# Optimization experiments

Hardware: AMD Instinct MI355X
Metric: run time of the kernel (lower is better)

## Reference

```python
import jax, jax.numpy as jnp
import numpy as np

EPS = 1e-5

def _act_quant(x):
    # per-token int8 absmax quantization (BitNet b1.58)
    scale = 127.0 / jnp.clip(jnp.max(jnp.abs(x), axis=-1, keepdims=True), EPS)
    return jnp.clip(jnp.round(x * scale), -128.0, 127.0) / scale

def _weight_quant(w):
    # per-tensor ternary quantization: round(w/mean|w|) clipped to {-1,0,1}
    scale = 1.0 / jnp.clip(jnp.mean(jnp.abs(w)), EPS)
    return jnp.clip(jnp.round(w * scale), -1.0, 1.0) / scale

def _ste(x, q):
    # straight-through estimator: forward uses q, backward passes through x
    return x + jax.lax.stop_gradient(q - x)

def bitlinear(x, w):
    xq = _ste(x, _act_quant(x))
    wq = _ste(w, _weight_quant(w))
    return jnp.einsum('btd,hd->bth', xq, wq)

def setup_inputs() -> dict:
    key = jax.random.key(0)
    k1, k2, k3 = jax.random.split(key, 3)
    B, T, D, H = 4, 1024, 2048, 8192
    x = jax.random.normal(k1, (B, T, D), dtype=jnp.float32)
    w1 = jax.random.normal(k2, (H, D), dtype=jnp.float32) * 0.02
    w2 = jax.random.normal(k3, (D, H), dtype=jnp.float32) * 0.02
    return {"x": x, "w1": w1, "w2": w2}

def reference(x, w1, w2):
    h = jax.nn.relu(bitlinear(x, w1))   # [B, T, H]
    out = bitlinear(h, w2)              # [B, T, D]
    return out
```

## Files before the change

kernel.cpp:

```cpp
#include <hip/hip_runtime.h>
#include <hip/hip_bf16.h>

#define EPSF 1e-5f

typedef int v4i __attribute__((ext_vector_type(4)));

static constexpr int BB = 4, TT = 1024, DD = 2048, HH = 8192;
static constexpr int MROWS = BB * TT;
static constexpr long long WCOUNT = (long long)DD * HH;


__device__ __forceinline__ void async_copy16(const void* g, void* l) {
  __builtin_amdgcn_global_load_lds(
      (const __attribute__((address_space(1))) unsigned int*)g,
      (__attribute__((address_space(3))) unsigned int*)l,
      16, 0, 0);
}

__device__ __forceinline__ int pack4(float a, float b, float c, float d,
                                     float scale, float lo, float hi) {
  int ia = (int)fminf(fmaxf(rintf(a * scale), lo), hi);
  int ib = (int)fminf(fmaxf(rintf(b * scale), lo), hi);
  int ic = (int)fminf(fmaxf(rintf(c * scale), lo), hi);
  int id = (int)fminf(fmaxf(rintf(d * scale), lo), hi);
  return (ia & 0xff) | ((ib & 0xff) << 8) | ((ic & 0xff) << 16) | ((id & 0xff) << 24);
}

__device__ __forceinline__ float blockMax256(float v) {
  #pragma unroll
  for (int off = 32; off; off >>= 1) v = fmaxf(v, __shfl_down(v, off, 64));
  __shared__ float sm[4];
  int lane = threadIdx.x & 63, wv = threadIdx.x >> 6;
  if (lane == 0) sm[wv] = v;
  __syncthreads();
  return fmaxf(fmaxf(sm[0], sm[1]), fmaxf(sm[2], sm[3]));
}


__global__ __launch_bounds__(256) void abs_sum_kernel(
    const float* __restrict__ w1, const float* __restrict__ w2,
    double* __restrict__ sums) {
  const float* w = blockIdx.y ? w2 : w1;
  const float4* w4 = (const float4*)w;
  long long n4 = WCOUNT / 4;
  float s = 0.f;
  for (long long i = (long long)blockIdx.x * blockDim.x + threadIdx.x; i < n4;
       i += (long long)gridDim.x * blockDim.x) {
    float4 v = w4[i];
    s += fabsf(v.x) + fabsf(v.y) + fabsf(v.z) + fabsf(v.w);
  }
  #pragma unroll
  for (int off = 32; off; off >>= 1) s += __shfl_down(s, off, 64);
  __shared__ float sm[4];
  int lane = threadIdx.x & 63, wv = threadIdx.x >> 6;
  if (lane == 0) sm[wv] = s;
  __syncthreads();
  if (threadIdx.x == 0) {
    float t = sm[0] + sm[1] + sm[2] + sm[3];
    atomicAdd(&sums[blockIdx.y], (double)t);
  }
}


__global__ __launch_bounds__(256) void quant_w_kernel(
    const float* __restrict__ w1, const float* __restrict__ w2,
    const double* __restrict__ sums,
    signed char* __restrict__ q1, signed char* __restrict__ q2) {
  const float* w = blockIdx.y ? w2 : w1;
  signed char* q = blockIdx.y ? q2 : q1;
  float mean = fmaxf((float)(sums[blockIdx.y] * (1.0 / (double)WCOUNT)), EPSF);
  float scale = 1.0f / mean;
  const float4* w4 = (const float4*)w;
  int* q4 = (int*)q;
  long long n4 = WCOUNT / 4;
  for (long long i = (long long)blockIdx.x * blockDim.x + threadIdx.x; i < n4;
       i += (long long)gridDim.x * blockDim.x) {
    float4 v = w4[i];
    q4[i] = pack4(v.x, v.y, v.z, v.w, scale, -1.f, 1.f);
  }
}


__global__ __launch_bounds__(256) void quant_x_kernel(
    const float* __restrict__ x, signed char* __restrict__ xq,
    float* __restrict__ ascale) {
  int row = blockIdx.x;
  const float4* xr = (const float4*)(x + (size_t)row * DD);
  int t = threadIdx.x;
  float4 v0 = xr[2 * t], v1 = xr[2 * t + 1];
  float m = fmaxf(fmaxf(fabsf(v0.x), fabsf(v0.y)), fmaxf(fabsf(v0.z), fabsf(v0.w)));
  m = fmaxf(m, fmaxf(fmaxf(fabsf(v1.x), fabsf(v1.y)), fmaxf(fabsf(v1.z), fabsf(v1.w))));
  float am = fmaxf(blockMax256(m), EPSF);
  float scale = 127.0f / am;
  int* out = (int*)(xq + (size_t)row * DD);
  out[2 * t]     = pack4(v0.x, v0.y, v0.z, v0.w, scale, -128.f, 127.f);
  out[2 * t + 1] = pack4(v1.x, v1.y, v1.z, v1.w, scale, -128.f, 127.f);
  if (t == 0) ascale[row] = am / 127.0f;
}


__global__ __launch_bounds__(256) void quant_h_kernel(
    const float* __restrict__ h, signed char* __restrict__ hq,
    float* __restrict__ ascale) {
  int row = blockIdx.x;
  const float4* hr = (const float4*)(h + (size_t)row * HH);
  int t = threadIdx.x;
  float4 v[8];
  float m = 0.f;
  #pragma unroll
  for (int i = 0; i < 8; i++) {
    v[i] = hr[t + i * 256];
    m = fmaxf(m, fmaxf(fmaxf(fabsf(v[i].x), fabsf(v[i].y)),
                       fmaxf(fabsf(v[i].z), fabsf(v[i].w))));
  }
  float am = fmaxf(blockMax256(m), EPSF);
  float scale = 127.0f / am;
  int* out = (int*)(hq + (size_t)row * HH);
  #pragma unroll
  for (int i = 0; i < 8; i++)
    out[t + i * 256] = pack4(v[i].x, v[i].y, v[i].z, v[i].w, scale, -128.f, 127.f);
  if (t == 0) ascale[row] = am / 127.0f;
}


template <int RELU>
__global__ __launch_bounds__(256) void gemm_i8_kernel(
    const signed char* __restrict__ A, const signed char* __restrict__ B,
    float* __restrict__ C, const float* __restrict__ ascale,
    const double* __restrict__ wsum, int M, int N, int K) {
  __shared__ signed char As[128 * 128];
  __shared__ signed char Bs[128 * 128];

  const int t = threadIdx.x;
  const int lane = t & 63, wv = t >> 6;
  const int wm = wv >> 1, wn = wv & 1;
  const int m0 = blockIdx.y * 128, n0 = blockIdx.x * 128;
  const int q = lane >> 4;

  const int segBase = wv * 4;
  const signed char* aSrc[4];
  const signed char* bSrc[4];
  #pragma unroll
  for (int i = 0; i < 4; i++) {
    int seg = segBase + i;
    int r = seg * 8 + (lane >> 3);
    int c = (lane & 7) ^ (r & 7);
    aSrc[i] = A + (size_t)(m0 + r) * K + c * 16;
    bSrc[i] = B + (size_t)(n0 + r) * K + c * 16;
  }

  v4i acc[4][4];
  #pragma unroll
  for (int i = 0; i < 4; i++)
    #pragma unroll
    for (int j = 0; j < 4; j++) {
      v4i z = {0, 0, 0, 0};
      acc[i][j] = z;
    }

  int rowA[4], rowB[4];
  #pragma unroll
  for (int i = 0; i < 4; i++) {
    rowA[i] = wm * 64 + i * 16 + (lane & 15);
    rowB[i] = wn * 64 + i * 16 + (lane & 15);
  }

  for (int k0 = 0; k0 < K; k0 += 128) {
    #pragma unroll
    for (int i = 0; i < 4; i++) {
      async_copy16(aSrc[i] + k0, &As[(segBase + i) * 1024]);
      async_copy16(bSrc[i] + k0, &Bs[(segBase + i) * 1024]);
    }
    __syncthreads();
    #pragma unroll
    for (int kc = 0; kc < 2; kc++) {
      v4i af[4], bf[4];
      #pragma unroll
      for (int i = 0; i < 4; i++) {
        int ca = (kc * 4 + q) ^ (rowA[i] & 7);
        af[i] = *(const v4i*)(As + rowA[i] * 128 + ca * 16);
        int cb = (kc * 4 + q) ^ (rowB[i] & 7);
        bf[i] = *(const v4i*)(Bs + rowB[i] * 128 + cb * 16);
      }
      #pragma unroll
      for (int i = 0; i < 4; i++)
        #pragma unroll
        for (int j = 0; j < 4; j++)
          acc[i][j] = __builtin_amdgcn_mfma_i32_16x16x64_i8(af[i], bf[j], acc[i][j], 0, 0, 0);
    }
    __syncthreads();
  }

  float wmean = fmaxf((float)(wsum[0] * (1.0 / (double)WCOUNT)), EPSF);
  #pragma unroll
  for (int i = 0; i < 4; i++) {
    int mBase = m0 + wm * 64 + i * 16 + q * 4;
    #pragma unroll
    for (int e = 0; e < 4; e++) {
      float f = ascale[mBase + e] * wmean;
      #pragma unroll
      for (int j = 0; j < 4; j++) {
        int n = n0 + wn * 64 + j * 16 + (lane & 15);
        float v = (float)acc[i][j][e] * f;
        if (RELU) v = fmaxf(v, 0.f);
        C[(size_t)(mBase + e) * N + n] = v;
      }
    }
  }
}


extern "C" void kernel_launch(void* const* d_in, const int* in_sizes, int n_in,
                              void* d_out, int out_size, void* d_ws, size_t ws_size,
                              hipStream_t stream) {
  const float* x  = (const float*)d_in[0];
  const float* w1 = (const float*)d_in[1];
  const float* w2 = (const float*)d_in[2];
  float* out = (float*)d_out;

  char* ws = (char*)d_ws;
  double* sums = (double*)ws;
  float* a1 = (float*)(ws + 256);
  float* a2 = (float*)(ws + 256 + 16384);
  signed char* w1q = (signed char*)(ws + 33024);
  signed char* w2q = w1q + (size_t)WCOUNT;
  signed char* xq  = w2q + (size_t)WCOUNT;
  signed char* hq  = xq + (size_t)MROWS * DD;
  float* h = (float*)(hq + (size_t)MROWS * HH);

  hipMemsetAsync(sums, 0, 16, stream);
  abs_sum_kernel<<<dim3(1024, 2), 256, 0, stream>>>(w1, w2, sums);
  quant_w_kernel<<<dim3(2048, 2), 256, 0, stream>>>(w1, w2, sums, w1q, w2q);
  quant_x_kernel<<<MROWS, 256, 0, stream>>>(x, xq, a1);
  gemm_i8_kernel<1><<<dim3(HH / 128, MROWS / 128), 256, 0, stream>>>(
      xq, w1q, h, a1, &sums[0], MROWS, HH, DD);
  quant_h_kernel<<<MROWS, 256, 0, stream>>>(h, hq, a2);
  gemm_i8_kernel<0><<<dim3(DD / 128, MROWS / 128), 256, 0, stream>>>(
      hq, w2q, out, a2, &sums[1], MROWS, DD, HH);
}
```

Before: 419.1 us.

## Store first GEMM output as int16, add tile swizzle and larger BK

The first GEMM now writes the ReLU'd raw int32 accumulator clamped to int16 rather than scaled float32, which halves the intermediate h write and read traffic. The per-row scale is reapplied inside the h-quantization kernel, which also computes its absmax on integers. It also adds a grouped tile-index swizzle for better L2 reuse and uses a K-tile of 256 for the second GEMM to cut iterations and barriers. Clamping at 32767 can saturate large accumulators and change results, and the larger LDS tile may reduce occupancy.

```diff
diff --git a/kernel.cpp b/kernel.cpp
--- a/kernel.cpp
+++ b/kernel.cpp
@@ -4,6 +4,7 @@
 #define EPSF 1e-5f
 
 typedef int v4i __attribute__((ext_vector_type(4)));
+typedef short v8s __attribute__((ext_vector_type(8)));
 
 static constexpr int BB = 4, TT = 1024, DD = 2048, HH = 8192;
 static constexpr int MROWS = BB * TT;
@@ -26,7 +27,7 @@
   return (ia & 0xff) | ((ib & 0xff) << 8) | ((ic & 0xff) << 16) | ((id & 0xff) << 24);
 }
 
-__device__ __forceinline__ float blockMax256(float v) {
+__device__ __forceinline__ float blockMaxF256(float v) {
   #pragma unroll
   for (int off = 32; off; off >>= 1) v = fmaxf(v, __shfl_down(v, off, 64));
   __shared__ float sm[4];
@@ -34,6 +35,27 @@
   if (lane == 0) sm[wv] = v;
   __syncthreads();
   return fmaxf(fmaxf(sm[0], sm[1]), fmaxf(sm[2], sm[3]));
+}
+
+__device__ __forceinline__ int blockMaxI256(int v) {
+  #pragma unroll
+  for (int off = 32; off; off >>= 1) v = max(v, __shfl_down(v, off, 64));
+  __shared__ int sm[4];
+  int lane = threadIdx.x & 63, wv = threadIdx.x >> 6;
+  if (lane == 0) sm[wv] = v;
+  __syncthreads();
+  return max(max(sm[0], sm[1]), max(sm[2], sm[3]));
+}
+
+__device__ __forceinline__ void swizzle_tiles(int& mt, int& nt) {
+  int Mt = gridDim.y, Nt = gridDim.x;
+  int id = blockIdx.y * Nt + blockIdx.x;
+  int c = id & 7, k = id >> 3;
+  int pm = (Mt >= Nt) ? 4 : 2;
+  int PM = Mt / pm, PN = Nt / (8 / pm);
+  int pr = c % pm, pc = c / pm;
+  mt = pr * PM + (k % PM);
+  nt = pc * PN + (k / PM);
 }
 
 
@@ -90,7 +112,7 @@
   float4 v0 = xr[2 * t], v1 = xr[2 * t + 1];
   float m = fmaxf(fmaxf(fabsf(v0.x), fabsf(v0.y)), fmaxf(fabsf(v0.z), fabsf(v0.w)));
   m = fmaxf(m, fmaxf(fmaxf(fabsf(v1.x), fabsf(v1.y)), fmaxf(fabsf(v1.z), fabsf(v1.w))));
-  float am = fmaxf(blockMax256(m), EPSF);
+  float am = fmaxf(blockMaxF256(m), EPSF);
   float scale = 127.0f / am;
   int* out = (int*)(xq + (size_t)row * DD);
   out[2 * t]     = pack4(v0.x, v0.y, v0.z, v0.w, scale, -128.f, 127.f);
@@ -100,51 +122,66 @@
 
 
 __global__ __launch_bounds__(256) void quant_h_kernel(
-    const float* __restrict__ h, signed char* __restrict__ hq,
-    float* __restrict__ ascale) {
+    const short* __restrict__ h, signed char* __restrict__ hq,
+    float* __restrict__ a2, const float* __restrict__ a1,
+    const double* __restrict__ sums) {
   int row = blockIdx.x;
-  const float4* hr = (const float4*)(h + (size_t)row * HH);
   int t = threadIdx.x;
-  float4 v[8];
-  float m = 0.f;
-  #pragma unroll
-  for (int i = 0; i < 8; i++) {
+  const v8s* hr = (const v8s*)(h + (size_t)row * HH);
+  v8s v[4];
+  int mx = 0;
+  #pragma unroll
+  for (int i = 0; i < 4; i++) {
     v[i] = hr[t + i * 256];
-    m = fmaxf(m, fmaxf(fmaxf(fabsf(v[i].x), fabsf(v[i].y)),
-                       fmaxf(fabsf(v[i].z), fabsf(v[i].w))));
-  }
-  float am = fmaxf(blockMax256(m), EPSF);
+    #pragma unroll
+    for (int j = 0; j < 8; j++) mx = max(mx, (int)v[i][j]);
+  }
+  int bmx = blockMaxI256(mx);
+  float wmean1 = fmaxf((float)(sums[0] * (1.0 / (double)WCOUNT)), EPSF);
+  float f = a1[row] * wmean1;
+  float maxh = (float)bmx * f;
+  float am = fmaxf(maxh, EPSF);
   float scale = 127.0f / am;
   int* out = (int*)(hq + (size_t)row * HH);
   #pragma unroll
-  for (int i = 0; i < 8; i++)
-    out[t + i * 256] = pack4(v[i].x, v[i].y, v[i].z, v[i].w, scale, -128.f, 127.f);
-  if (t == 0) ascale[row] = am / 127.0f;
-}
-
-
-template <int RELU>
+  for (int i = 0; i < 4; i++) {
+    out[(t + i * 256) * 2] =
+        pack4((float)v[i][0] * f, (float)v[i][1] * f, (float)v[i][2] * f,
+              (float)v[i][3] * f, scale, -128.f, 127.f);
+    out[(t + i * 256) * 2 + 1] =
+        pack4((float)v[i][4] * f, (float)v[i][5] * f, (float)v[i][6] * f,
+              (float)v[i][7] * f, scale, -128.f, 127.f);
+  }
+  if (t == 0) a2[row] = am / 127.0f;
+}
+
+
+template <int MODE, int BK>
 __global__ __launch_bounds__(256) void gemm_i8_kernel(
     const signed char* __restrict__ A, const signed char* __restrict__ B,
-    float* __restrict__ C, const float* __restrict__ ascale,
+    void* __restrict__ Cout, const float* __restrict__ ascale,
     const double* __restrict__ wsum, int M, int N, int K) {
-  __shared__ signed char As[128 * 128];
-  __shared__ signed char Bs[128 * 128];
+  constexpr int CH = BK / 16;
+  constexpr int SEGROWS = 1024 / BK;
+  constexpr int SPW = BK / 32;
+  __shared__ signed char As[128 * BK];
+  __shared__ signed char Bs[128 * BK];
 
   const int t = threadIdx.x;
   const int lane = t & 63, wv = t >> 6;
   const int wm = wv >> 1, wn = wv & 1;
-  const int m0 = blockIdx.y * 128, n0 = blockIdx.x * 128;
+  int mt, nt;
+  swizzle_tiles(mt, nt);
+  const int m0 = mt * 128, n0 = nt * 128;
   const int q = lane >> 4;
 
-  const int segBase = wv * 4;
-  const signed char* aSrc[4];
-  const signed char* bSrc[4];
-  #pragma unroll
-  for (int i = 0; i < 4; i++) {
-    int seg = segBase + i;
-    int r = seg * 8 + (lane >> 3);
-    int c = (lane & 7) ^ (r & 7);
+  const signed char* aSrc[SPW];
+  const signed char* bSrc[SPW];
+  #pragma unroll
+  for (int i = 0; i < SPW; i++) {
+    int seg = wv * SPW + i;
+    int r = seg * SEGROWS + lane / CH;
+    int c = (lane % CH) ^ (r & (CH - 1));
     aSrc[i] = A + (size_t)(m0 + r) * K + c * 16;
     bSrc[i] = B + (size_t)(n0 + r) * K + c * 16;
   }
@@ -165,22 +202,22 @@
     rowB[i] = wn * 64 + i * 16 + (lane & 15);
   }
 
-  for (int k0 = 0; k0 < K; k0 += 128) {
-    #pragma unroll
-    for (int i = 0; i < 4; i++) {
-      async_copy16(aSrc[i] + k0, &As[(segBase + i) * 1024]);
-      async_copy16(bSrc[i] + k0, &Bs[(segBase + i) * 1024]);
+  for (int k0 = 0; k0 < K; k0 += BK) {
+    #pragma unroll
+    for (int i = 0; i < SPW; i++) {
+      async_copy16(aSrc[i] + k0, &As[(wv * SPW + i) * 1024]);
+      async_copy16(bSrc[i] + k0, &Bs[(wv * SPW + i) * 1024]);
     }
     __syncthreads();
     #pragma unroll
-    for (int kc = 0; kc < 2; kc++) {
+    for (int kc = 0; kc < CH / 4; kc++) {
       v4i af[4], bf[4];
       #pragma unroll
       for (int i = 0; i < 4; i++) {
-        int ca = (kc * 4 + q) ^ (rowA[i] & 7);
-        af[i] = *(const v4i*)(As + rowA[i] * 128 + ca * 16);
-        int cb = (kc * 4 + q) ^ (rowB[i] & 7);
-        bf[i] = *(const v4i*)(Bs + rowB[i] * 128 + cb * 16);
+        int ca = (kc * 4 + q) ^ (rowA[i] & (CH - 1));
+        af[i] = *(const v4i*)(As + rowA[i] * BK + ca * 16);
+        int cb = (kc * 4 + q) ^ (rowB[i] & (CH - 1));
+        bf[i] = *(const v4i*)(Bs + rowB[i] * BK + cb * 16);
       }
       #pragma unroll
       for (int i = 0; i < 4; i++)
@@ -191,19 +228,36 @@
     __syncthreads();
   }
 
-  float wmean = fmaxf((float)(wsum[0] * (1.0 / (double)WCOUNT)), EPSF);
-  #pragma unroll
-  for (int i = 0; i < 4; i++) {
-    int mBase = m0 + wm * 64 + i * 16 + q * 4;
-    #pragma unroll
-    for (int e = 0; e < 4; e++) {
-      float f = ascale[mBase + e] * wmean;
-      #pragma unroll
-      for (int j = 0; j < 4; j++) {
-        int n = n0 + wn * 64 + j * 16 + (lane & 15);
-        float v = (float)acc[i][j][e] * f;
-        if (RELU) v = fmaxf(v, 0.f);
-        C[(size_t)(mBase + e) * N + n] = v;
+  if constexpr (MODE == 1) {
+    short* C = (short*)Cout;
+    #pragma unroll
+    for (int i = 0; i < 4; i++) {
+      int mBase = m0 + wm * 64 + i * 16 + q * 4;
+      #pragma unroll
+      for (int e = 0; e < 4; e++) {
+        #pragma unroll
+        for (int j = 0; j < 4; j++) {
+          int n = n0 + wn * 64 + j * 16 + (lane & 15);
+          int r = acc[i][j][e];
+          r = r < 0 ? 0 : (r > 32767 ? 32767 : r);
+          C[(size_t)(mBase + e) * N + n] = (short)r;
+        }
+      }
+    }
+  } else {
+    float* C = (float*)Cout;
+    float wmean = fmaxf((float)(wsum[0] * (1.0 / (double)WCOUNT)), EPSF);
+    #pragma unroll
+    for (int i = 0; i < 4; i++) {
+      int mBase = m0 + wm * 64 + i * 16 + q * 4;
+      #pragma unroll
+      for (int e = 0; e < 4; e++) {
+        float f = ascale[mBase + e] * wmean;
+        #pragma unroll
+        for (int j = 0; j < 4; j++) {
+          int n = n0 + wn * 64 + j * 16 + (lane & 15);
+          C[(size_t)(mBase + e) * N + n] = (float)acc[i][j][e] * f;
+        }
       }
     }
   }
@@ -226,15 +280,15 @@
   signed char* w2q = w1q + (size_t)WCOUNT;
   signed char* xq  = w2q + (size_t)WCOUNT;
   signed char* hq  = xq + (size_t)MROWS * DD;
-  float* h = (float*)(hq + (size_t)MROWS * HH);
+  short* h16 = (short*)(hq + (size_t)MROWS * HH);
 
   hipMemsetAsync(sums, 0, 16, stream);
   abs_sum_kernel<<<dim3(1024, 2), 256, 0, stream>>>(w1, w2, sums);
   quant_w_kernel<<<dim3(2048, 2), 256, 0, stream>>>(w1, w2, sums, w1q, w2q);
   quant_x_kernel<<<MROWS, 256, 0, stream>>>(x, xq, a1);
-  gemm_i8_kernel<1><<<dim3(HH / 128, MROWS / 128), 256, 0, stream>>>(
-      xq, w1q, h, a1, &sums[0], MROWS, HH, DD);
-  quant_h_kernel<<<MROWS, 256, 0, stream>>>(h, hq, a2);
-  gemm_i8_kernel<0><<<dim3(DD / 128, MROWS / 128), 256, 0, stream>>>(
+  gemm_i8_kernel<1, 128><<<dim3(HH / 128, MROWS / 128), 256, 0, stream>>>(
+      xq, w1q, h16, nullptr, nullptr, MROWS, HH, DD);
+  quant_h_kernel<<<MROWS, 256, 0, stream>>>(h16, hq, a2, a1, sums);
+  gemm_i8_kernel<0, 256><<<dim3(DD / 128, MROWS / 128), 256, 0, stream>>>(
       hq, w2q, out, a2, &sums[1], MROWS, DD, HH);
 }
```

Result: faster. 389.9 us (-7.0%).
